# Kernel optimization log

Hardware: AMD Instinct MI355X
Metric: run time of the kernel (lower is better)

The kernel has to match this reference:

```python
import jax, jax.numpy as jnp
import numpy as np

TAO = 3
M = 5
C_IN = 7
D_MODEL = 512
KERNELS = D_MODEL // C_IN          # 73
EXTRA = D_MODEL - C_IN * KERNELS   # 1


def _circular_conv1d(x_nct, w_oik, b_o):
    # Conv1d(kernel_size=3, padding=1, padding_mode='circular') == wrap-pad by 1 then VALID conv.
    xp = jnp.pad(x_nct, ((0, 0), (0, 0), (1, 1)), mode='wrap')
    out = jax.lax.conv_general_dilated(
        xp, w_oik, window_strides=(1,), padding='VALID',
        dimension_numbers=('NCH', 'OIH', 'NCH'))
    return out + b_o[None, :, None]


def setup_inputs() -> dict:
    key = jax.random.key(0)
    k1, k2, k3 = jax.random.split(key, 3)
    B, S = 32, 4096
    x = jax.random.normal(k1, (B, S, C_IN), dtype=jnp.float32)
    # kaiming_normal fan_in for Conv1d(in=m+1, k=3): std = sqrt(2/(1+0.01**2)) / sqrt((M+1)*3)
    std = float(np.sqrt(2.0 / (1.0 + 0.01 ** 2)) / np.sqrt((M + 1) * 3))
    w_conv = jax.random.normal(k2, (KERNELS, M + 1, 3), dtype=jnp.float32) * std
    b_conv = jnp.zeros((KERNELS,), dtype=jnp.float32)
    w_left = jax.random.normal(k3, (EXTRA, M + 1, 3), dtype=jnp.float32) * std
    b_left = jnp.zeros((EXTRA,), dtype=jnp.float32)
    return {"x": x, "w_conv": w_conv, "b_conv": b_conv, "w_left": w_left, "b_left": b_left}


def reference(x, w_conv, b_conv, w_left, b_left):
    B, S, C = x.shape
    L = S - M * TAO
    # time-delay gather: faithful vectors [x[t], x[t-tao], ..., x[t-m*tao]] per channel
    valid_t = jnp.arange(M * TAO, S)
    offs = jnp.arange(M + 1) * TAO
    idx = valid_t[:, None] - offs[None, :]            # [L, m+1]
    ext = x[:, idx, :]                                # [B, L, m+1, C]
    ext = jnp.transpose(ext, (0, 1, 3, 2))            # [B, L, C, m+1] (channel-major)
    emb = ext.reshape(B, L, C * (M + 1))
    emb = jnp.pad(emb, ((0, 0), (M * TAO, 0), (0, 0)))  # pad=True: left-pad time with zeros -> [B,S,C*(m+1)]
    # split into c_in chunks of (m+1) and run the SAME conv on each -> batch over (B*C)
    chunks = emb.reshape(B, S, C, M + 1).transpose(0, 2, 3, 1)  # [B, C, m+1, S]
    merged = chunks.reshape(B * C, M + 1, S)
    out = _circular_conv1d(merged, w_conv, b_conv)              # [B*C, K, S]
    out = out.reshape(B, C * KERNELS, S)                        # concat of per-chunk outputs
    # leftout conv on the LAST chunk only
    last = chunks[:, -1]                                        # [B, m+1, S]
    out_left = _circular_conv1d(last, w_left, b_left)           # [B, extra, S]
    out_full = jnp.concatenate([out, out_left], axis=1)         # [B, d_model, S]
    return jnp.transpose(out_full, (0, 2, 1))                   # [B, S, d_model]
```

## Files before the change

kernel.cpp:

```cpp
#include <hip/hip_runtime.h>

#define S      4096
#define CIN    7
#define DM     512
#define KERN   73
#define TT     256
#define TILES  (S / TT)
#define NSTAGE (TT + 17)
#define TROW   292
#define CHUNK  32
#define NCH    (TT / CHUNK)

__device__ __forceinline__ void do_chunk32(const float* __restrict__ xc,
                                           const float g[18], float bias,
                                           float* __restrict__ opc)
{
    float acc[CHUNK];
    #pragma unroll
    for (int i = 0; i < CHUNK; ++i) acc[i] = bias;

    #pragma unroll
    for (int q = 0; q < 13; ++q) {
        float4 v = *reinterpret_cast<const float4*>(xc + 4 * q);
        float va[4] = {v.x, v.y, v.z, v.w};
        #pragma unroll
        for (int e = 0; e < 4; ++e) {
            const int j = 4 * q + e;
            #pragma unroll
            for (int i = 0; i < CHUNK; ++i) {
                const int off = j - i;
                if (off >= 0 && off < 18)
                    acc[i] = fmaf(g[off], va[e], acc[i]);
            }
        }
        if (q >= 4 && q < 12) {
            const int lo = (q == 4) ? 0 : (4 * q - 17);
            const int hi = 4 * q - 14;
            #pragma unroll
            for (int i = 0; i < CHUNK; ++i)
                if (i >= lo && i <= hi) opc[i * DM] = acc[i];
        }
        if (q == 12) {
            #pragma unroll
            for (int i = 31; i <= 31; ++i) opc[i * DM] = acc[i];
        }
    }
}

__global__ __launch_bounds__(512, 2)
void tokemb_kernel(const float* __restrict__ x,
                   const float* __restrict__ w_conv,
                   const float* __restrict__ b_conv,
                   const float* __restrict__ w_left,
                   const float* __restrict__ b_left,
                   float* __restrict__ out)
{
    __shared__ float xs[CIN * TROW];

    const int blk  = blockIdx.x;
    const int b    = blk / TILES;
    const int tile = blk & (TILES - 1);
    const int t0   = tile * TT;
    const int tid  = threadIdx.x;

    {
        const float* xb = x + (long long)b * S * CIN;
        const long long base = (long long)(t0 - 16) * CIN;
        const int nfl = CIN * NSTAGE;
        for (int e4 = 4 * tid; e4 < nfl; e4 += 4 * 512) {
            long long src = base + e4;
            if (src >= 0 && src + 3 < (long long)S * CIN) {
                float4 v = *reinterpret_cast<const float4*>(xb + src);
                float va[4] = {v.x, v.y, v.z, v.w};
                #pragma unroll
                for (int u = 0; u < 4; ++u) {
                    int e = e4 + u;
                    int j = e / CIN, c = e - j * CIN;
                    xs[c * TROW + j] = va[u];
                }
            } else {
                #pragma unroll
                for (int u = 0; u < 4; ++u) {
                    int e = e4 + u;
                    if (e < nfl) {
                        int j = e / CIN, c = e - j * CIN;
                        int tm = t0 - 16 + j;
                        if (tm < 0) tm += S; else if (tm >= S) tm -= S;
                        xs[c * TROW + j] = xb[tm * CIN + c];
                    }
                }
            }
        }
    }

    const int d  = tid;
    const int oo = d % KERN;
    const float* wrow = (d < DM - 1) ? (w_conv + oo * 18) : w_left;
    const float bias  = (d < DM - 1) ? b_conv[oo] : b_left[0];
    const int cc = (d < DM - 1) ? (d / KERN) : (CIN - 1);
    float g[18];
    #pragma unroll
    for (int off = 0; off < 18; ++off)
        g[off] = wrow[(5 - off / 3) * 3 + (off % 3)];

    __syncthreads();

    const float* xrow = xs + cc * TROW;
    float* const op = out + ((long long)b * S + t0) * DM + d;

    const int wid = tid >> 6;
    const bool edgetile = (tile == 0) || (tile == TILES - 1);

    for (int cc_ = 0; cc_ < NCH; ++cc_) {
        const int ch  = (cc_ + wid) & (NCH - 1);
        const int jb  = ch * CHUNK;
        const int tc  = t0 + jb;
        float* opc = op + jb * DM;

        if (!edgetile || !((tc < 16) || (tc + CHUNK >= S))) {
            do_chunk32(xrow + jb, g, bias, opc);
        } else {
            #pragma unroll
            for (int i = 0; i < CHUNK; ++i) {
                float p0 = 0.f, p1 = 0.f, p2 = 0.f;
                #pragma unroll
                for (int o = 0; o < 18; o += 3) {
                    p0 = fmaf(g[o],     xrow[jb + i + o],     p0);
                    p1 = fmaf(g[o + 1], xrow[jb + i + o + 1], p1);
                    p2 = fmaf(g[o + 2], xrow[jb + i + o + 2], p2);
                }
                const int t = tc + i;
                const float f0 = (t == 0 || t >= 16)     ? 1.f : 0.f;
                const float f1 = (t >= 15)               ? 1.f : 0.f;
                const float f2 = (t >= 14 && t != S - 1) ? 1.f : 0.f;
                opc[i * DM] = bias + f0 * p0 + f1 * p1 + f2 * p2;
            }
        }
    }
}

extern "C" void kernel_launch(void* const* d_in, const int* in_sizes, int n_in,
                              void* d_out, int out_size, void* d_ws, size_t ws_size,
                              hipStream_t stream) {
    const float* x      = (const float*)d_in[0];
    const float* w_conv = (const float*)d_in[1];
    const float* b_conv = (const float*)d_in[2];
    const float* w_left = (const float*)d_in[3];
    const float* b_left = (const float*)d_in[4];
    float* out = (float*)d_out;

    const int B = in_sizes[0] / (S * CIN);
    dim3 grid(B * TILES);
    tokemb_kernel<<<grid, 512, 0, stream>>>(x, w_conv, b_conv, w_left, b_left, out);
}
```

Baseline: 48.59 us.

## Compute two adjacent output channels per thread with float2 stores

Each thread now computes two consecutive output channels, and the 512 threads are split into two groups that each cover half of the tile's time chunks. The results go out as float2 stores, which halves the number of store instructions and widens each global write. The cost is roughly double the accumulator and weight registers (64 accumulators plus 36 weights), which under launch_bounds(512,2) risks spilling. When the two channels sit on different input rows, the paired LDS reads stop being shared broadcasts.

```diff
diff --git a/kernel.cpp b/kernel.cpp
--- a/kernel.cpp
+++ b/kernel.cpp
@@ -11,26 +11,32 @@
 #define CHUNK  32
 #define NCH    (TT / CHUNK)
 
-__device__ __forceinline__ void do_chunk32(const float* __restrict__ xc,
-                                           const float g[18], float bias,
-                                           float* __restrict__ opc)
+__device__ __forceinline__ void do_chunk32_pair(const float* __restrict__ x0,
+                                                const float* __restrict__ x1,
+                                                const float g0[18], const float g1[18],
+                                                float bias0, float bias1,
+                                                float* __restrict__ opc)
 {
-    float acc[CHUNK];
+    float a0[CHUNK], a1[CHUNK];
     #pragma unroll
-    for (int i = 0; i < CHUNK; ++i) acc[i] = bias;
+    for (int i = 0; i < CHUNK; ++i) { a0[i] = bias0; a1[i] = bias1; }
 
     #pragma unroll
     for (int q = 0; q < 13; ++q) {
-        float4 v = *reinterpret_cast<const float4*>(xc + 4 * q);
-        float va[4] = {v.x, v.y, v.z, v.w};
+        float4 v0 = *reinterpret_cast<const float4*>(x0 + 4 * q);
+        float4 v1 = *reinterpret_cast<const float4*>(x1 + 4 * q);
+        float va0[4] = {v0.x, v0.y, v0.z, v0.w};
+        float va1[4] = {v1.x, v1.y, v1.z, v1.w};
         #pragma unroll
         for (int e = 0; e < 4; ++e) {
             const int j = 4 * q + e;
             #pragma unroll
             for (int i = 0; i < CHUNK; ++i) {
                 const int off = j - i;
-                if (off >= 0 && off < 18)
-                    acc[i] = fmaf(g[off], va[e], acc[i]);
+                if (off >= 0 && off < 18) {
+                    a0[i] = fmaf(g0[off], va0[e], a0[i]);
+                    a1[i] = fmaf(g1[off], va1[e], a1[i]);
+                }
             }
         }
         if (q >= 4 && q < 12) {
@@ -38,11 +44,14 @@
             const int hi = 4 * q - 14;
             #pragma unroll
             for (int i = 0; i < CHUNK; ++i)
-                if (i >= lo && i <= hi) opc[i * DM] = acc[i];
+                if (i >= lo && i <= hi) {
+                    float2 w = make_float2(a0[i], a1[i]);
+                    *reinterpret_cast<float2*>(opc + i * DM) = w;
+                }
         }
         if (q == 12) {
-            #pragma unroll
-            for (int i = 31; i <= 31; ++i) opc[i * DM] = acc[i];
+            float2 w = make_float2(a0[31], a1[31]);
+            *reinterpret_cast<float2*>(opc + 31 * DM) = w;
         }
     }
 }
@@ -93,47 +102,60 @@
         }
     }
 
-    const int d  = tid;
-    const int oo = d % KERN;
-    const float* wrow = (d < DM - 1) ? (w_conv + oo * 18) : w_left;
-    const float bias  = (d < DM - 1) ? b_conv[oo] : b_left[0];
-    const int cc = (d < DM - 1) ? (d / KERN) : (CIN - 1);
-    float g[18];
+    const int pid = tid & 255;
+    const int tg  = tid >> 8;
+    const int d0  = 2 * pid;
+
+    float g[2][18], bias[2];
+    const float* xr[2];
     #pragma unroll
-    for (int off = 0; off < 18; ++off)
-        g[off] = wrow[(5 - off / 3) * 3 + (off % 3)];
+    for (int dd = 0; dd < 2; ++dd) {
+        const int d  = d0 + dd;
+        const int oo = d % KERN;
+        const float* wrow = (d < DM - 1) ? (w_conv + oo * 18) : w_left;
+        bias[dd] = (d < DM - 1) ? b_conv[oo] : b_left[0];
+        const int cc = (d < DM - 1) ? (d / KERN) : (CIN - 1);
+        xr[dd] = xs + cc * TROW;
+        #pragma unroll
+        for (int off = 0; off < 18; ++off)
+            g[dd][off] = wrow[(5 - off / 3) * 3 + (off % 3)];
+    }
 
     __syncthreads();
 
-    const float* xrow = xs + cc * TROW;
-    float* const op = out + ((long long)b * S + t0) * DM + d;
+    float* const op = out + ((long long)b * S + t0) * DM + d0;
 
     const int wid = tid >> 6;
     const bool edgetile = (tile == 0) || (tile == TILES - 1);
 
-    for (int cc_ = 0; cc_ < NCH; ++cc_) {
-        const int ch  = (cc_ + wid) & (NCH - 1);
+    for (int cc_ = 0; cc_ < 4; ++cc_) {
+        const int ch  = tg * 4 + ((cc_ + wid) & 3);
         const int jb  = ch * CHUNK;
         const int tc  = t0 + jb;
         float* opc = op + jb * DM;
 
         if (!edgetile || !((tc < 16) || (tc + CHUNK >= S))) {
-            do_chunk32(xrow + jb, g, bias, opc);
+            do_chunk32_pair(xr[0] + jb, xr[1] + jb, g[0], g[1],
+                            bias[0], bias[1], opc);
         } else {
             #pragma unroll
-            for (int i = 0; i < CHUNK; ++i) {
-                float p0 = 0.f, p1 = 0.f, p2 = 0.f;
+            for (int dd = 0; dd < 2; ++dd) {
+                const float* xw = xr[dd] + jb;
                 #pragma unroll
-                for (int o = 0; o < 18; o += 3) {
-                    p0 = fmaf(g[o],     xrow[jb + i + o],     p0);
-                    p1 = fmaf(g[o + 1], xrow[jb + i + o + 1], p1);
-                    p2 = fmaf(g[o + 2], xrow[jb + i + o + 2], p2);
+                for (int i = 0; i < CHUNK; ++i) {
+                    float p0 = 0.f, p1 = 0.f, p2 = 0.f;
+                    #pragma unroll
+                    for (int o = 0; o < 18; o += 3) {
+                        p0 = fmaf(g[dd][o],     xw[i + o],     p0);
+                        p1 = fmaf(g[dd][o + 1], xw[i + o + 1], p1);
+                        p2 = fmaf(g[dd][o + 2], xw[i + o + 2], p2);
+                    }
+                    const int t = tc + i;
+                    const float f0 = (t == 0 || t >= 16)     ? 1.f : 0.f;
+                    const float f1 = (t >= 15)               ? 1.f : 0.f;
+                    const float f2 = (t >= 14 && t != S - 1) ? 1.f : 0.f;
+                    opc[i * DM + dd] = bias[dd] + f0 * p0 + f1 * p1 + f2 * p2;
                 }
-                const int t = tc + i;
-                const float f0 = (t == 0 || t >= 16)     ? 1.f : 0.f;
-                const float f1 = (t >= 15)               ? 1.f : 0.f;
-                const float f2 = (t >= 14 && t != S - 1) ? 1.f : 0.f;
-                opc[i * DM] = bias + f0 * p0 + f1 * p1 + f2 * p2;
             }
         }
     }
```

After: 54.40 us. +12.0%, slower.
